# Kernel tuning notes

Hardware: AMD Instinct MI355X
Metric: run time of the kernel (lower is better)

The kernel has to match this reference:

```python
import jax, jax.numpy as jnp
import numpy as np

B, S, IN, OUT = 4, 2048, 4096, 1024
ROUNDS = 12  # prime_factors(4096) == [2]*12
QMIN, QMAX = -128, 127


def _create_noise(key, shape, lo, hi):
    # Obfuscation noise spanning the data range; exactly corrected in forward.
    return jax.random.uniform(key, shape, jnp.float32, -0.5, 0.5) * (hi - lo)


def setup_inputs() -> dict:
    key = jax.random.key(0)
    ks = jax.random.split(key, 6)
    x = jax.random.normal(ks[0], (B, S, IN), jnp.float32)
    weight = jax.random.normal(ks[1], (OUT, IN), jnp.float32) * 0.02
    bias = jax.random.normal(ks[2], (OUT,), jnp.float32) * 0.02
    weight_noise = _create_noise(ks[3], (OUT, IN), weight.min(), weight.max())
    noise_x = _create_noise(ks[4], (B, S, IN), x.min(), x.max())
    # one random permutation of in_features per round
    perms = jnp.stack([jax.random.permutation(jax.random.fold_in(key, 1000 + r), IN)
                       for r in range(ROUNDS)]).astype(jnp.int32)
    # 2048 random orthogonal 2x2 blocks per round (rotations, like ortho_group with dim=2)
    theta = jax.random.uniform(ks[5], (ROUNDS, IN // 2), jnp.float32, 0.0, 2.0 * np.pi)
    c, s = jnp.cos(theta), jnp.sin(theta)
    row0 = jnp.stack([c, -s], axis=-1)
    row1 = jnp.stack([s, c], axis=-1)
    matrices = jnp.stack([row0, row1], axis=-2)  # (ROUNDS, IN//2, 2, 2)
    return {"x": x, "weight": weight, "bias": bias, "weight_noise": weight_noise,
            "noise_x": noise_x, "permutations": perms, "matrices": matrices}


def _permute_matrix_operation(X, perms, mats):
    # X: (..., n, cols). Each round: gather rows by permutation, then apply a
    # block-diagonal orthogonal transform (G blocks of size f along the n axis).
    lead = X.shape[:-2]
    n, cols = X.shape[-2], X.shape[-1]
    G, f = mats.shape[1], mats.shape[2]
    for r in range(mats.shape[0]):
        X = jnp.take(X, perms[r], axis=-2)
        Xb = X.reshape(lead + (G, f, cols))
        X = jnp.einsum('gij,...gjc->...gic', mats[r], Xb).reshape(lead + (n, cols))
    return X


def _quant_dequant(t):
    # Asymmetric per-tensor quantize -> round -> clamp -> dequantize (int8-style).
    lo, hi = t.min(), t.max()
    scale = (hi - lo) / (QMAX - QMIN)
    zp = jnp.round(QMIN - lo / scale)
    q = jnp.clip(jnp.round(t / scale + zp), QMIN, QMAX)
    return (q - zp) * scale


def reference(x, weight, bias, weight_noise, noise_x, permutations, matrices):
    # inverse-transpose blocks; equals `matrices` for orthogonal blocks, kept explicit for fidelity
    inv_mats_mT = jnp.swapaxes(jnp.linalg.inv(matrices), -1, -2)
    w_plus = weight + weight_noise                                   # (OUT, IN)
    permuted_w = jnp.swapaxes(
        _permute_matrix_operation(jnp.swapaxes(w_plus, -1, -2), permutations, inv_mats_mT), -1, -2)
    qw = _quant_dequant(permuted_w)                                  # (OUT, IN)
    permuted_x = jnp.swapaxes(
        _permute_matrix_operation(jnp.swapaxes(x + noise_x, -1, -2), permutations, matrices), -1, -2)
    qx = _quant_dequant(permuted_x)                                  # (B, S, IN)
    res = qx @ qw.T + bias                                           # quantized matmul + bias
    res = res - x @ weight_noise.T                                   # correction term 1
    res = res - noise_x @ w_plus.T                                   # correction term 2
    return res
```

## Files before the change

kernel.cpp:

```cpp
#include <hip/hip_runtime.h>


#define IN_F   4096
#define OUT_F  1024
#define MROWS  8192
#define KTOT   12288
#define KHALF  6144
#define NPASS  6

typedef _Float16 f16;
typedef _Float16 f16x8 __attribute__((ext_vector_type(8)));
typedef _Float16 f16x4 __attribute__((ext_vector_type(4)));
typedef float    f32x4 __attribute__((ext_vector_type(4)));

#define OFF_XT  (0ull)
#define OFF_WT  (OFF_XT + (size_t)MROWS * IN_F * 4)
#define OFF_A   (OFF_WT + (size_t)OUT_F * IN_F * 4)
#define OFF_B   (OFF_A + (size_t)MROWS * KTOT * 2)
#define OFF_MM  (OFF_B + (size_t)OUT_F * KTOT * 2)
#define OFF_TIX (OFF_MM + 256)
#define OFF_TCX (OFF_TIX + (size_t)NPASS * 2048 * 8)
#define OFF_TIW (OFF_TCX + (size_t)NPASS * 2048 * 32)
#define OFF_TCW (OFF_TIW + (size_t)NPASS * 2048 * 8)

__device__ __forceinline__ unsigned enc_f(float f) {
  unsigned u = __float_as_uint(f);
  return (u & 0x80000000u) ? ~u : (u | 0x80000000u);
}
__device__ __forceinline__ float dec_f(unsigned u) {
  unsigned b = (u & 0x80000000u) ? (u & 0x7fffffffu) : ~u;
  return __uint_as_float(b);
}

__global__ void build_tables_kernel(const int* __restrict__ perms,
                                    const float* __restrict__ mats,
                                    uint2* __restrict__ tIx, float4* __restrict__ tCx,
                                    uint2* __restrict__ tIw, float4* __restrict__ tCw,
                                    unsigned* __restrict__ mm) {
  if (blockIdx.x == 0 && threadIdx.x == 0) {
    mm[0] = 0xFFFFFFFFu; mm[1] = 0u; mm[2] = 0xFFFFFFFFu; mm[3] = 0u;
  }
  int p = blockIdx.x;
  int r0 = 2 * p, r1 = 2 * p + 1;
  for (int g = threadIdx.x; g < 2048; g += blockDim.x) {
    int q0 = perms[r1 * IN_F + 2 * g], q1 = perms[r1 * IN_F + 2 * g + 1];
    int a0 = q0 >> 1, e0 = q0 & 1, a1 = q1 >> 1, e1 = q1 & 1;
    unsigned i0 = perms[r0 * IN_F + 2 * a0], i1 = perms[r0 * IN_F + 2 * a0 + 1];
    unsigned i2 = perms[r0 * IN_F + 2 * a1], i3 = perms[r0 * IN_F + 2 * a1 + 1];
    uint2 idx = make_uint2(i0 | (i1 << 16), i2 | (i3 << 16));
    const float* Ma = mats + ((size_t)r0 * 2048 + a0) * 4;
    const float* Mb = mats + ((size_t)r0 * 2048 + a1) * 4;
    const float* M1 = mats + ((size_t)r1 * 2048 + g) * 4;
    int o = p * 2048 + g;
    {
      float c00 = Ma[e0 * 2], c01 = Ma[e0 * 2 + 1];
      float c10 = Mb[e1 * 2], c11 = Mb[e1 * 2 + 1];
      float m00 = M1[0], m01 = M1[1], m10 = M1[2], m11 = M1[3];
      tIx[o] = idx;
      tCx[2 * o]     = make_float4(m00 * c00, m00 * c01, m01 * c10, m01 * c11);
      tCx[2 * o + 1] = make_float4(m10 * c00, m10 * c01, m11 * c10, m11 * c11);
    }
    {
      float rda = 1.0f / (Ma[0] * Ma[3] - Ma[1] * Ma[2]);
      float rdb = 1.0f / (Mb[0] * Mb[3] - Mb[1] * Mb[2]);
      float rd1 = 1.0f / (M1[0] * M1[3] - M1[1] * M1[2]);
      float c00 = (e0 == 0 ? Ma[3] : -Ma[1]) * rda;
      float c01 = (e0 == 0 ? -Ma[2] : Ma[0]) * rda;
      float c10 = (e1 == 0 ? Mb[3] : -Mb[1]) * rdb;
      float c11 = (e1 == 0 ? -Mb[2] : Mb[0]) * rdb;
      float m00 = M1[3] * rd1, m01 = -M1[2] * rd1;
      float m10 = -M1[1] * rd1, m11 = M1[0] * rd1;
      tIw[o] = idx;
      tCw[2 * o]     = make_float4(m00 * c00, m00 * c01, m01 * c10, m01 * c11);
      tCw[2 * o + 1] = make_float4(m10 * c00, m10 * c01, m11 * c10, m11 * c11);
    }
  }
}

__global__ __launch_bounds__(1024) void transform_kernel(
    const float* __restrict__ x, const float* __restrict__ nx,
    const float* __restrict__ w, const float* __restrict__ wn,
    const uint2* __restrict__ tIx, const float4* __restrict__ tCx,
    const uint2* __restrict__ tIw, const float4* __restrict__ tCw,
    float* __restrict__ xt, float* __restrict__ wt,
    f16* __restrict__ Aall, f16* __restrict__ Ball,
    unsigned* __restrict__ mm) {
  __shared__ float2 buf[2][IN_F];
  const int t = threadIdx.x;
  const bool isW = blockIdx.x >= (MROWS / 2);
  const float *in0, *in1; const uint2* tI; const float4* tC;
  float* tout; f16* fout; int mmidx; size_t m0;
  if (!isW) {
    m0 = (size_t)blockIdx.x * 2;
    in0 = x; in1 = nx; tI = tIx; tC = tCx; tout = xt; fout = Aall; mmidx = 0;
  } else {
    m0 = (size_t)(blockIdx.x - MROWS / 2) * 2;
    in0 = w; in1 = wn; tI = tIw; tC = tCw; tout = wt; fout = Ball; mmidx = 2;
  }
  f16* f0 = fout + m0 * KTOT;
  f16* f1 = fout + (m0 + 1) * KTOT;

  {
    float4 a0 = ((const float4*)(in0 + m0 * IN_F))[t];
    float4 b0 = ((const float4*)(in1 + m0 * IN_F))[t];
    float4 a1 = ((const float4*)(in0 + (m0 + 1) * IN_F))[t];
    float4 b1 = ((const float4*)(in1 + (m0 + 1) * IN_F))[t];
    float4 s0 = make_float4(a0.x + b0.x, a0.y + b0.y, a0.z + b0.z, a0.w + b0.w);
    float4 s1 = make_float4(a1.x + b1.x, a1.y + b1.y, a1.z + b1.z, a1.w + b1.w);
    int c = t * 4;
    *(float4*)&buf[0][c]     = make_float4(s0.x, s1.x, s0.y, s1.y);
    *(float4*)&buf[0][c + 2] = make_float4(s0.z, s1.z, s0.w, s1.w);
    f16x4 p0, p1, q0, q1;
    if (isW) {
      p0.x=(f16)b0.x; p0.y=(f16)b0.y; p0.z=(f16)b0.z; p0.w=(f16)b0.w;
      q0.x=(f16)s0.x; q0.y=(f16)s0.y; q0.z=(f16)s0.z; q0.w=(f16)s0.w;
      p1.x=(f16)b1.x; p1.y=(f16)b1.y; p1.z=(f16)b1.z; p1.w=(f16)b1.w;
      q1.x=(f16)s1.x; q1.y=(f16)s1.y; q1.z=(f16)s1.z; q1.w=(f16)s1.w;
    } else {
      p0.x=(f16)(-a0.x); p0.y=(f16)(-a0.y); p0.z=(f16)(-a0.z); p0.w=(f16)(-a0.w);
      q0.x=(f16)(-b0.x); q0.y=(f16)(-b0.y); q0.z=(f16)(-b0.z); q0.w=(f16)(-b0.w);
      p1.x=(f16)(-a1.x); p1.y=(f16)(-a1.y); p1.z=(f16)(-a1.z); p1.w=(f16)(-a1.w);
      q1.x=(f16)(-b1.x); q1.y=(f16)(-b1.y); q1.z=(f16)(-b1.z); q1.w=(f16)(-b1.w);
    }
    *(f16x4*)(f0 + IN_F + c)     = p0;
    *(f16x4*)(f0 + 2 * IN_F + c) = q0;
    *(f16x4*)(f1 + IN_F + c)     = p1;
    *(f16x4*)(f1 + 2 * IN_F + c) = q1;
  }
  __syncthreads();

  int cur = 0;
  for (int pass = 0; pass < NPASS; pass++) {
    const uint2* ti = tI + pass * 2048;
    const float4* tc = tC + (size_t)pass * 4096;
#pragma unroll
    for (int i = 0; i < 2; i++) {
      int g = i * 1024 + t;
      uint2 pk = ti[g];
      float4 cA = tc[2 * g], cB = tc[2 * g + 1];
      float2 x0 = buf[cur][pk.x & 0xffff], x1 = buf[cur][pk.x >> 16];
      float2 x2 = buf[cur][pk.y & 0xffff], x3 = buf[cur][pk.y >> 16];
      float y0x = cA.x * x0.x + cA.y * x1.x + cA.z * x2.x + cA.w * x3.x;
      float y0y = cA.x * x0.y + cA.y * x1.y + cA.z * x2.y + cA.w * x3.y;
      float y1x = cB.x * x0.x + cB.y * x1.x + cB.z * x2.x + cB.w * x3.x;
      float y1y = cB.x * x0.y + cB.y * x1.y + cB.z * x2.y + cB.w * x3.y;
      *(float4*)&buf[cur ^ 1][2 * g] = make_float4(y0x, y0y, y1x, y1y);
    }
    cur ^= 1;
    __syncthreads();
  }
  float lmin = 3.4e38f, lmax = -3.4e38f;
  {
    int c = t * 4;
    float4 q0 = *(float4*)&buf[0][c];
    float4 q1 = *(float4*)&buf[0][c + 2];
    ((float4*)(tout + m0 * IN_F))[t]       = make_float4(q0.x, q0.z, q1.x, q1.z);
    ((float4*)(tout + (m0 + 1) * IN_F))[t] = make_float4(q0.y, q0.w, q1.y, q1.w);
    lmin = fminf(fminf(fminf(q0.x, q0.y), fminf(q0.z, q0.w)),
                 fminf(fminf(q1.x, q1.y), fminf(q1.z, q1.w)));
    lmax = fmaxf(fmaxf(fmaxf(q0.x, q0.y), fmaxf(q0.z, q0.w)),
                 fmaxf(fmaxf(q1.x, q1.y), fmaxf(q1.z, q1.w)));
  }
#pragma unroll
  for (int off = 32; off > 0; off >>= 1) {
    lmin = fminf(lmin, __shfl_down(lmin, off));
    lmax = fmaxf(lmax, __shfl_down(lmax, off));
  }
  float* red = (float*)&buf[1][0];
  int wid = t >> 6;
  if ((t & 63) == 0) { red[wid * 2] = lmin; red[wid * 2 + 1] = lmax; }
  __syncthreads();
  if (t == 0) {
    float bmin = red[0], bmax = red[1];
#pragma unroll
    for (int i = 1; i < 16; i++) {
      bmin = fminf(bmin, red[i * 2]);
      bmax = fmaxf(bmax, red[i * 2 + 1]);
    }
    atomicMin(&mm[mmidx], enc_f(bmin));
    atomicMax(&mm[mmidx + 1], enc_f(bmax));
  }
}

__global__ void finalize_kernel(unsigned* mm) {
  float* sc = (float*)(mm + 4);
  float xlo = dec_f(mm[0]), xhi = dec_f(mm[1]);
  float wlo = dec_f(mm[2]), whi = dec_f(mm[3]);
  float sx = (xhi - xlo) / 255.0f;
  float zx = rintf(-128.0f - xlo / sx);
  float sw = (whi - wlo) / 255.0f;
  float zw = rintf(-128.0f - wlo / sw);
  sc[0] = sx; sc[1] = zx; sc[2] = sw; sc[3] = zw;
}

__global__ __launch_bounds__(256) void quant_kernel(
    const float* __restrict__ xt, const float* __restrict__ wt,
    f16* __restrict__ Aall, f16* __restrict__ Ball,
    const unsigned* __restrict__ mm) {
  const float* sc = (const float*)(mm + 4);
  const bool isW = blockIdx.x >= MROWS;
  int m = isW ? blockIdx.x - MROWS : blockIdx.x;
  float s = isW ? sc[2] : sc[0], zp = isW ? sc[3] : sc[1];
  const float4* srow = (const float4*)((isW ? wt : xt) + (size_t)m * IN_F);
  f16* drow = (isW ? Ball : Aall) + (size_t)m * KTOT;
  int t = threadIdx.x;
#pragma unroll
  for (int j = 0; j < 4; j++) {
    int i4 = j * 256 + t;
    float4 v = srow[i4];
    float q0 = (fminf(fmaxf(rintf(v.x / s + zp), -128.f), 127.f) - zp) * s;
    float q1 = (fminf(fmaxf(rintf(v.y / s + zp), -128.f), 127.f) - zp) * s;
    float q2 = (fminf(fmaxf(rintf(v.z / s + zp), -128.f), 127.f) - zp) * s;
    float q3 = (fminf(fmaxf(rintf(v.w / s + zp), -128.f), 127.f) - zp) * s;
    f16x4 o; o.x = (f16)q0; o.y = (f16)q1; o.z = (f16)q2; o.w = (f16)q3;
    *(f16x4*)(drow + i4 * 4) = o;
  }
}

__global__ __launch_bounds__(256) void bias_init_kernel(
    const float* __restrict__ bias, float* __restrict__ out) {
  const float4* b4 = (const float4*)bias;
  float4* o4 = (float4*)out;
  int idx = blockIdx.x * 256 + threadIdx.x;
  const int total = MROWS * OUT_F / 4;
  for (int i = idx; i < total; i += gridDim.x * 256)
    o4[i] = b4[i & (OUT_F / 4 - 1)];
}

__device__ __forceinline__ void gl2lds16(const void* g, void* l) {
  __builtin_amdgcn_global_load_lds(
      (__attribute__((address_space(1))) void*)g,
      (__attribute__((address_space(3))) void*)l, 16, 0, 0);
}

__global__ __launch_bounds__(256, 4) void gemm_kernel(
    const f16* __restrict__ A, const f16* __restrict__ B,
    float* __restrict__ out) {
  __shared__ f16 As[128 * 32];
  __shared__ f16 Bs[128 * 32];
  const int tid = threadIdx.x;
  const int wave = tid >> 6, lane = tid & 63;
  const int quad = lane >> 4, fr = lane & 15;
  const int bm = blockIdx.x & 63;
  const int bn = (blockIdx.x >> 6) & 7;
  const int ks = blockIdx.x >> 9;
  const int k0 = ks * KHALF;
  const int wm = (wave & 1) * 64, wn = (wave >> 1) * 64;

  f32x4 acc[4][4] = {};

  const int l4 = lane >> 2;
  const int lc = (lane & 3) * 8;
  const size_t arow = (size_t)(bm * 128 + wave * 16 + l4);
  const size_t brow = (size_t)(bn * 128 + wave * 16 + l4);
  const f16* ag0 = A + arow * KTOT + k0 + lc;
  const f16* ag1 = A + (arow + 64) * KTOT + k0 + lc;
  const f16* bg0 = B + brow * KTOT + k0 + lc;
  const f16* bg1 = B + (brow + 64) * KTOT + k0 + lc;
  f16* as0 = As + (wave * 16) * 32;
  f16* as1 = As + (64 + wave * 16) * 32;
  f16* bs0 = Bs + (wave * 16) * 32;
  f16* bs1 = Bs + (64 + wave * 16) * 32;

  for (int kk = 0; kk < KHALF; kk += 32) {
    gl2lds16(ag0 + kk, as0);
    gl2lds16(ag1 + kk, as1);
    gl2lds16(bg0 + kk, bs0);
    gl2lds16(bg1 + kk, bs1);
    __syncthreads();
    f16x8 af[4], bf[4];
#pragma unroll
    for (int mi = 0; mi < 4; mi++)
      af[mi] = *(const f16x8*)(As + (wm + mi * 16 + fr) * 32 + quad * 8);
#pragma unroll
    for (int ni = 0; ni < 4; ni++)
      bf[ni] = *(const f16x8*)(Bs + (wn + ni * 16 + fr) * 32 + quad * 8);
#pragma unroll
    for (int mi = 0; mi < 4; mi++)
#pragma unroll
      for (int ni = 0; ni < 4; ni++)
        acc[mi][ni] = __builtin_amdgcn_mfma_f32_16x16x32_f16(
            af[mi], bf[ni], acc[mi][ni], 0, 0, 0);
    __syncthreads();
  }

#pragma unroll
  for (int mi = 0; mi < 4; mi++) {
    int gm = bm * 128 + wm + mi * 16 + quad * 4;
#pragma unroll
    for (int ni = 0; ni < 4; ni++) {
      int gn = bn * 128 + wn + ni * 16 + fr;
#pragma unroll
      for (int e = 0; e < 4; e++)
        unsafeAtomicAdd(&out[(size_t)(gm + e) * OUT_F + gn], acc[mi][ni][e]);
    }
  }
}

extern "C" void kernel_launch(void* const* d_in, const int* in_sizes, int n_in,
                              void* d_out, int out_size, void* d_ws, size_t ws_size,
                              hipStream_t stream) {
  const float* x     = (const float*)d_in[0];
  const float* w     = (const float*)d_in[1];
  const float* bias  = (const float*)d_in[2];
  const float* wn    = (const float*)d_in[3];
  const float* nx    = (const float*)d_in[4];
  const int*   perms = (const int*)d_in[5];
  const float* mats  = (const float*)d_in[6];
  float* out = (float*)d_out;

  char* ws = (char*)d_ws;
  float* xt   = (float*)(ws + OFF_XT);
  float* wt   = (float*)(ws + OFF_WT);
  f16*   Aall = (f16*)(ws + OFF_A);
  f16*   Ball = (f16*)(ws + OFF_B);
  unsigned* mm = (unsigned*)(ws + OFF_MM);
  uint2*  tIx = (uint2*)(ws + OFF_TIX);
  float4* tCx = (float4*)(ws + OFF_TCX);
  uint2*  tIw = (uint2*)(ws + OFF_TIW);
  float4* tCw = (float4*)(ws + OFF_TCW);

  build_tables_kernel<<<NPASS, 256, 0, stream>>>(perms, mats, tIx, tCx, tIw, tCw, mm);
  transform_kernel<<<MROWS / 2 + OUT_F / 2, 1024, 0, stream>>>(
      x, nx, w, wn, tIx, tCx, tIw, tCw, xt, wt, Aall, Ball, mm);
  finalize_kernel<<<1, 1, 0, stream>>>(mm);
  quant_kernel<<<MROWS + OUT_F, 256, 0, stream>>>(xt, wt, Aall, Ball, mm);
  bias_init_kernel<<<1024, 256, 0, stream>>>(bias, out);
  gemm_kernel<<<2 * (MROWS / 128) * (OUT_F / 128), 256, 0, stream>>>(Aall, Ball, out);
}
```

Baseline: 731.8 us.

## Rewrite GEMM with 256x256 tiles, double-buffered LDS pipeline and swizzled layout

Replaces the 128x128 single-buffered GEMM with a 512-thread, 256x256-tile kernel. It uses double-buffered 128KB dynamic LDS, XOR-swizzled shared layout, staged global-to-LDS prefetch interleaved with MFMA quadrants, s_setprio hints and a block-index remap for L2 locality. This is meant to cut redundant global traffic and hide load latency behind compute that the old kernel exposed at every k-step. The risks are lower occupancy from the large LDS footprint, and synchronisation correctness with the manual vmcnt waits and barriers.

```diff
diff --git a/kernel.cpp b/kernel.cpp
--- a/kernel.cpp
+++ b/kernel.cpp
@@ -7,6 +7,7 @@
 #define KTOT   12288
 #define KHALF  6144
 #define NPASS  6
+#define NTIL   96
 
 typedef _Float16 f16;
 typedef _Float16 f16x8 __attribute__((ext_vector_type(8)));
@@ -233,68 +234,154 @@
       (__attribute__((address_space(3))) void*)l, 16, 0, 0);
 }
 
-__global__ __launch_bounds__(256, 4) void gemm_kernel(
+#define GBAR() asm volatile("s_barrier" ::: "memory")
+#define MFMA16(d, va, vb) d = __builtin_amdgcn_mfma_f32_16x16x32_f16(va, vb, d, 0, 0, 0)
+
+#define STAGE(t, hh) do {                                                   \
+    const int c_ = (t) & 1;                                                 \
+    if ((hh) < 2) {                                                         \
+      const f16* g_ = gA + (size_t)((hh) * 128) * KTOT + (size_t)(t) * 64;  \
+      f16* l_ = As + c_ * 16384 + (hh) * 8192 + sbase;                      \
+      gl2lds16(g_, l_);                                                     \
+      gl2lds16(g_ + (size_t)64 * KTOT, l_ + 4096);                          \
+    } else {                                                                \
+      const f16* g_ = gB + (size_t)(((hh) - 2) * 128) * KTOT + (size_t)(t) * 64; \
+      f16* l_ = Bs + c_ * 16384 + ((hh) - 2) * 8192 + sbase;                \
+      gl2lds16(g_, l_);                                                     \
+      gl2lds16(g_ + (size_t)64 * KTOT, l_ + 4096);                          \
+    }                                                                       \
+  } while (0)
+
+__global__ __launch_bounds__(512, 2) void gemm_kernel(
     const f16* __restrict__ A, const f16* __restrict__ B,
     float* __restrict__ out) {
-  __shared__ f16 As[128 * 32];
-  __shared__ f16 Bs[128 * 32];
+  extern __shared__ f16 sm[];
+  f16* As = sm;
+  f16* Bs = sm + 32768;
+
   const int tid = threadIdx.x;
   const int wave = tid >> 6, lane = tid & 63;
-  const int quad = lane >> 4, fr = lane & 15;
-  const int bm = blockIdx.x & 63;
-  const int bn = (blockIdx.x >> 6) & 7;
-  const int ks = blockIdx.x >> 9;
-  const int k0 = ks * KHALF;
-  const int wm = (wave & 1) * 64, wn = (wave >> 1) * 64;
-
-  f32x4 acc[4][4] = {};
-
-  const int l4 = lane >> 2;
-  const int lc = (lane & 3) * 8;
-  const size_t arow = (size_t)(bm * 128 + wave * 16 + l4);
-  const size_t brow = (size_t)(bn * 128 + wave * 16 + l4);
-  const f16* ag0 = A + arow * KTOT + k0 + lc;
-  const f16* ag1 = A + (arow + 64) * KTOT + k0 + lc;
-  const f16* bg0 = B + brow * KTOT + k0 + lc;
-  const f16* bg1 = B + (brow + 64) * KTOT + k0 + lc;
-  f16* as0 = As + (wave * 16) * 32;
-  f16* as1 = As + (64 + wave * 16) * 32;
-  f16* bs0 = Bs + (wave * 16) * 32;
-  f16* bs1 = Bs + (64 + wave * 16) * 32;
-
-  for (int kk = 0; kk < KHALF; kk += 32) {
-    gl2lds16(ag0 + kk, as0);
-    gl2lds16(ag1 + kk, as1);
-    gl2lds16(bg0 + kk, bs0);
-    gl2lds16(bg1 + kk, bs1);
-    __syncthreads();
-    f16x8 af[4], bf[4];
-#pragma unroll
-    for (int mi = 0; mi < 4; mi++)
-      af[mi] = *(const f16x8*)(As + (wm + mi * 16 + fr) * 32 + quad * 8);
+  const int fr = lane & 15, quad = lane >> 4;
+  const int wm = wave >> 2, wn = wave & 3;
+
+  const int orig = blockIdx.x;
+  const int wg = (orig & 7) * 32 + (orig >> 3);
+  const int ks = wg >> 7;
+  const int rem = wg & 127;
+  const int bn = rem >> 5, bm = rem & 31;
+  const size_t k0 = (size_t)ks * KHALF;
+
+  const int srow = (wave << 3) + (lane >> 3);
+  const int scol = ((lane & 7) << 3) ^ ((srow & 4) << 2);
+  const f16* gA = A + ((size_t)bm * 256 + srow) * KTOT + k0 + scol;
+  const f16* gB = B + ((size_t)bn * 256 + srow) * KTOT + k0 + scol;
+  const int sbase = wave << 9;
+
+  const int rdoff = fr * 64 + ((quad << 3) ^ ((fr & 4) << 2));
+  const f16* rA = As + wm * 8192 + rdoff;
+  const f16* rB = Bs + (wn >> 1) * 8192 + (wn & 1) * 4096 + rdoff;
+
+  f16x8 a0[4][2], a1[4][2], bF[4][2];
+  f32x4 acc[8][4] = {};
+
+  STAGE(0, 0); STAGE(0, 1); STAGE(0, 2); STAGE(0, 3);
+  STAGE(1, 0); STAGE(1, 1);
+  asm volatile("s_waitcnt vmcnt(4)" ::: "memory");
+  GBAR();
+
+  for (int t = 0; t < NTIL; ++t) {
+    const int c = t & 1;
+    const f16* pa = rA + c * 16384;
+    const f16* pb = rB + c * 16384;
+
+#pragma unroll
+    for (int i = 0; i < 4; i++) {
+      a0[i][0] = *(const f16x8*)(pa + i * 1024);
+      a0[i][1] = *(const f16x8*)(pa + i * 1024 + 32);
+    }
+#pragma unroll
+    for (int j = 0; j < 2; j++) {
+      bF[j][0] = *(const f16x8*)(pb + j * 1024);
+      bF[j][1] = *(const f16x8*)(pb + j * 1024 + 32);
+    }
+    if (t + 1 < NTIL) STAGE(t + 1, 2);
+    GBAR();
+    __builtin_amdgcn_s_setprio(1);
+#pragma unroll
+    for (int i = 0; i < 4; i++)
+#pragma unroll
+      for (int j = 0; j < 2; j++) {
+        MFMA16(acc[i][j], a0[i][0], bF[j][0]);
+        MFMA16(acc[i][j], a0[i][1], bF[j][1]);
+      }
+    __builtin_amdgcn_s_setprio(0);
+    GBAR();
+
+#pragma unroll
+    for (int i = 0; i < 4; i++) {
+      a1[i][0] = *(const f16x8*)(pa + (4 + i) * 1024);
+      a1[i][1] = *(const f16x8*)(pa + (4 + i) * 1024 + 32);
+    }
+#pragma unroll
+    for (int j = 0; j < 2; j++) {
+      bF[2 + j][0] = *(const f16x8*)(pb + (2 + j) * 1024);
+      bF[2 + j][1] = *(const f16x8*)(pb + (2 + j) * 1024 + 32);
+    }
+    if (t + 1 < NTIL) STAGE(t + 1, 3);
+    GBAR();
+    __builtin_amdgcn_s_setprio(1);
+#pragma unroll
+    for (int i = 0; i < 4; i++)
+#pragma unroll
+      for (int j = 0; j < 2; j++) {
+        MFMA16(acc[i][2 + j], a0[i][0], bF[2 + j][0]);
+        MFMA16(acc[i][2 + j], a0[i][1], bF[2 + j][1]);
+      }
+    __builtin_amdgcn_s_setprio(0);
+    GBAR();
+
+    if (t + 2 < NTIL) STAGE(t + 2, 0);
+    GBAR();
+    __builtin_amdgcn_s_setprio(1);
+#pragma unroll
+    for (int i = 0; i < 4; i++)
+#pragma unroll
+      for (int j = 0; j < 2; j++) {
+        MFMA16(acc[4 + i][j], a1[i][0], bF[j][0]);
+        MFMA16(acc[4 + i][j], a1[i][1], bF[j][1]);
+      }
+    __builtin_amdgcn_s_setprio(0);
+    GBAR();
+
+    if (t + 2 < NTIL) STAGE(t + 2, 1);
+    if (t + 2 < NTIL) {
+      asm volatile("s_waitcnt vmcnt(4)" ::: "memory");
+    } else if (t + 1 < NTIL) {
+      asm volatile("s_waitcnt vmcnt(0)" ::: "memory");
+    }
+    GBAR();
+    __builtin_amdgcn_s_setprio(1);
+#pragma unroll
+    for (int i = 0; i < 4; i++)
+#pragma unroll
+      for (int j = 0; j < 2; j++) {
+        MFMA16(acc[4 + i][2 + j], a1[i][0], bF[2 + j][0]);
+        MFMA16(acc[4 + i][2 + j], a1[i][1], bF[2 + j][1]);
+      }
+    __builtin_amdgcn_s_setprio(0);
+    GBAR();
+  }
+
+  const size_t orow = (size_t)bm * 256 + wm * 128 + quad * 4;
+  const int ocol = bn * 256 + wn * 64 + fr;
+#pragma unroll
+  for (int mi = 0; mi < 8; mi++)
 #pragma unroll
     for (int ni = 0; ni < 4; ni++)
-      bf[ni] = *(const f16x8*)(Bs + (wn + ni * 16 + fr) * 32 + quad * 8);
-#pragma unroll
-    for (int mi = 0; mi < 4; mi++)
-#pragma unroll
-      for (int ni = 0; ni < 4; ni++)
-        acc[mi][ni] = __builtin_amdgcn_mfma_f32_16x16x32_f16(
-            af[mi], bf[ni], acc[mi][ni], 0, 0, 0);
-    __syncthreads();
-  }
-
-#pragma unroll
-  for (int mi = 0; mi < 4; mi++) {
-    int gm = bm * 128 + wm + mi * 16 + quad * 4;
-#pragma unroll
-    for (int ni = 0; ni < 4; ni++) {
-      int gn = bn * 128 + wn + ni * 16 + fr;
 #pragma unroll
       for (int e = 0; e < 4; e++)
-        unsafeAtomicAdd(&out[(size_t)(gm + e) * OUT_F + gn], acc[mi][ni][e]);
-    }
-  }
+        unsafeAtomicAdd(&out[(orow + mi * 16 + e) * OUT_F + (ocol + ni * 16)],
+                        acc[mi][ni][e]);
 }
 
 extern "C" void kernel_launch(void* const* d_in, const int* in_sizes, int n_in,
@@ -320,11 +407,18 @@
   uint2*  tIw = (uint2*)(ws + OFF_TIW);
   float4* tCw = (float4*)(ws + OFF_TCW);
 
+  static int attr_set = 0;
+  if (!attr_set) {
+    (void)hipFuncSetAttribute(reinterpret_cast<const void*>(gemm_kernel),
+                              hipFuncAttributeMaxDynamicSharedMemorySize, 131072);
+    attr_set = 1;
+  }
+
   build_tables_kernel<<<NPASS, 256, 0, stream>>>(perms, mats, tIx, tCx, tIw, tCw, mm);
   transform_kernel<<<MROWS / 2 + OUT_F / 2, 1024, 0, stream>>>(
       x, nx, w, wn, tIx, tCx, tIw, tCw, xt, wt, Aall, Ball, mm);
   finalize_kernel<<<1, 1, 0, stream>>>(mm);
   quant_kernel<<<MROWS + OUT_F, 256, 0, stream>>>(xt, wt, Aall, Ball, mm);
   bias_init_kernel<<<1024, 256, 0, stream>>>(bias, out);
-  gemm_kernel<<<2 * (MROWS / 128) * (OUT_F / 128), 256, 0, stream>>>(Aall, Ball, out);
-}
+  gemm_kernel<<<2 * (MROWS / 256) * (OUT_F / 256), 512, 131072, stream>>>(Aall, Ball, out);
+}
```

Result: faster. 693.0 us (-5.3%).
